# Optimization experiments

Hardware: AMD Instinct MI355X
Metric: run time of the kernel (lower is better)

The kernel has to match this reference:

```python
import jax, jax.numpy as jnp
import numpy as np

B, I, H, T = 64, 128, 256, 1024


def setup_inputs() -> dict:
    key = jax.random.key(0)
    ks = jax.random.split(key, 18)
    stdv = 1.0 / np.sqrt(H)  # reset_parameters: uniform(-1/sqrt(hidden), 1/sqrt(hidden))
    u = lambda k, shape: jax.random.uniform(k, shape, jnp.float32, -stdv, stdv)
    return dict(
        X=jax.random.normal(ks[0], (B, I, T), jnp.float32),
        Mask=jax.random.randint(ks[1], (B, I, T), 0, 2).astype(jnp.float32),
        Delta=jax.random.uniform(ks[2], (B, I, T), jnp.float32),
        x_mean=jnp.float32(0.0),
        Wdgx=u(ks[3], (I, I)), bdgx=u(ks[4], (I,)),
        Wdgh=u(ks[5], (H, I)), bdgh=u(ks[6], (H,)),
        Wxz=u(ks[7], (H, I)), Whz=u(ks[8], (H, H)), Wmz=u(ks[9], (H, I)), bmz=u(ks[10], (H,)),
        Wxr=u(ks[11], (H, I)), Whr=u(ks[12], (H, H)), Wmr=u(ks[13], (H, I)),
        Wxh=u(ks[14], (H, I)), Whh=u(ks[15], (H, H)), Wmh=u(ks[16], (H, I)), bmh=u(ks[17], (H,)),
    )


def _grud(X, Mask, Delta, x_mean, Wdgx, bdgx, Wdgh, bdgh, Wxz, Whz, Wmz, bmz,
          Wxr, Whr, Wmr, Wxh, Whh, Wmh, bmh):
    # [B, I, T] -> time-major [T, B, I] for scan
    Xt = jnp.transpose(X, (2, 0, 1))
    Mt = jnp.transpose(Mask, (2, 0, 1))
    Dt = jnp.transpose(Delta, (2, 0, 1))

    def step(carry, xs):
        h, x_last = carry            # h: [B, H], x_last: [B, I]
        x, m, d = xs                 # each [B, I]
        gamma_x = jnp.exp(-jax.nn.relu(d @ Wdgx.T + bdgx))   # [B, I]
        gamma_h = jnp.exp(-jax.nn.relu(d @ Wdgh.T + bdgh))   # [B, H]
        x_last = jnp.where(m > 0, x, x_last)
        # faithful double imputation as in the torch source
        x1 = m * x + (1 - m) * (gamma_x * x + (1 - gamma_x) * x_mean)
        x2 = m * x1 + (1 - m) * (gamma_x * x_last + (1 - gamma_x) * x_mean)
        hd = gamma_h * h
        z = jax.nn.sigmoid(x2 @ Wxz.T + hd @ Whz.T + m @ Wmz.T + bmz)
        r = jax.nn.sigmoid(x2 @ Wxr.T + hd @ Whr.T + m @ Wmr.T)
        h_tilde = jnp.tanh(x2 @ Wxh.T + (r * hd) @ Whh.T + m @ Wmh.T + bmh)
        h_new = (1 - z) * hd + z * h_tilde
        return (h_new, x_last), h_new

    h0 = jnp.zeros((X.shape[0], Whz.shape[0]), X.dtype)      # Hidden_State buffer (zeros)
    xl0 = jnp.zeros((X.shape[0], X.shape[1]), X.dtype)       # X_last_obs buffer (zeros)
    _, hs = jax.lax.scan(step, (h0, xl0), (Xt, Mt, Dt))      # hs: [T, B, H]
    return jnp.transpose(hs, (1, 0, 2))                      # [B, T, H]


def reference(X, Mask, Delta, x_mean, Wdgx, bdgx, Wdgh, bdgh, Wxz, Whz, Wmz, bmz,
              Wxr, Whr, Wmr, Wxh, Whh, Wmh, bmh):
    return _grud(X, Mask, Delta, x_mean, Wdgx, bdgx, Wdgh, bdgh, Wxz, Whz, Wmz, bmz,
                 Wxr, Whr, Wmr, Wxh, Whh, Wmh, bmh)
```

## Files before the change

kernel.cpp:

```cpp
#include <hip/hip_runtime.h>
#include <cstdint>
#include <cstddef>

typedef _Float16 f16;
typedef _Float16 f16x8 __attribute__((ext_vector_type(8)));
typedef _Float16 f16x2 __attribute__((ext_vector_type(2)));
typedef float f32x4 __attribute__((ext_vector_type(4)));

#define B_ 64
#define I_ 128
#define H_ 256
#define T_ 1024
#define BT_ (B_*T_)

__device__ __forceinline__ uint32_t pack2_f16(float a, float b) {
  union { f16 h; uint16_t u; } ua, ub;
  ua.h = (f16)a; ub.h = (f16)b;
  return ((uint32_t)ub.u << 16) | (uint32_t)ua.u;
}

__device__ __forceinline__ float fdot2_u(uint32_t w, uint32_t x, float acc) {
  union { uint32_t u; f16x2 h; } uw, ux;
  uw.u = w; ux.u = x;
  return __builtin_amdgcn_fdot2(uw.h, ux.h, acc, false);
}

__device__ __forceinline__ float tanh_stable(float s) {
  float a = fabsf(s);
  float e = __expf(-2.f * a);
  float t = (1.f - e) * __fdividef(1.f, 1.f + e);
  return s < 0.f ? -t : t;
}

__device__ __forceinline__ float sigmoidf(float s) {
  return __fdividef(1.f, 1.f + __expf(-s));
}

__device__ __forceinline__ f16x8 load_frag(const f16* row, int k0, int g4) {
  union { uint32_t u[4]; f16x8 h; } r;
  const uint32_t* p0 = (const uint32_t*)(row + k0 + g4);
  const uint32_t* p1 = (const uint32_t*)(row + k0 + 16 + g4);
  r.u[0] = p0[0]; r.u[1] = p0[1];
  r.u[2] = p1[0]; r.u[3] = p1[1];
  return r.h;
}

__global__ void k_transpose_d(const float* __restrict__ D, f16* __restrict__ Dt) {
  __shared__ float tile[64][65];
  int t0 = blockIdx.x * 64, i0 = blockIdx.y * 64, b = blockIdx.z;
  int tx = threadIdx.x, ty = threadIdx.y;
  #pragma unroll
  for (int r = 0; r < 16; ++r) {
    int il = ty + r * 4;
    tile[il][tx] = D[((size_t)(b * I_ + i0 + il)) * T_ + t0 + tx];
  }
  __syncthreads();
  #pragma unroll
  for (int r = 0; r < 16; ++r) {
    int tl = ty + r * 4;
    Dt[((size_t)(b * T_ + t0 + tl)) * I_ + i0 + tx] = (f16)tile[tx][tl];
  }
}

__global__ void k_prep(const float* __restrict__ Wdgx, const float* __restrict__ bdgx,
                       const float* __restrict__ Wdgh, const float* __restrict__ bdgh,
                       const float* __restrict__ Wxz, const float* __restrict__ Whz,
                       const float* __restrict__ Wmz, const float* __restrict__ bmz,
                       const float* __restrict__ Wxr, const float* __restrict__ Whr,
                       const float* __restrict__ Wmr,
                       const float* __restrict__ Wxh, const float* __restrict__ Whh,
                       const float* __restrict__ Wmh, const float* __restrict__ bmh,
                       f16* __restrict__ Wg, float* __restrict__ bg,
                       f16* __restrict__ W3, float* __restrict__ b3,
                       uint32_t* __restrict__ blobR, uint32_t* __restrict__ blobZ,
                       uint32_t* __restrict__ blobH) {
  int tid = blockIdx.x * blockDim.x + threadIdx.x;
  int nth = gridDim.x * blockDim.x;
  for (int idx = tid; idx < 384 * 128; idx += nth) {
    int j = idx >> 7, k = idx & 127;
    float v = (j < 128) ? Wdgx[j * 128 + k] : Wdgh[(j - 128) * 128 + k];
    Wg[idx] = (f16)v;
  }
  for (int j = tid; j < 384; j += nth) bg[j] = (j < 128) ? bdgx[j] : bdgh[j - 128];
  for (int idx = tid; idx < 768 * 256; idx += nth) {
    int j = idx >> 8, c = idx & 255;
    const float* Wx = (j < 256) ? Wxz : ((j < 512) ? Wxr : Wxh);
    const float* Wm = (j < 256) ? Wmz : ((j < 512) ? Wmr : Wmh);
    int jj = j & 255;
    float v = (c < 128) ? Wx[jj * 128 + c] : Wm[jj * 128 + (c - 128)];
    W3[idx] = (f16)v;
  }
  for (int j = tid; j < 768; j += nth)
    b3[j] = (j < 256) ? bmz[j] : ((j < 512) ? 0.0f : bmh[j - 512]);
  for (int idx = tid; idx < 64 * 512; idx += nth) {
    int c = idx >> 9, th = idx & 511;
    int rr = c >> 5, cc = c & 31;
    int ks = th >> 7, rg = th & 127;
    int row = rg * 2 + rr;
    int k = ks * 64 + cc * 2;
    blobR[idx] = pack2_f16(Whr[row * 256 + k], Whr[row * 256 + k + 1]);
    blobZ[idx] = pack2_f16(Whz[row * 256 + k], Whz[row * 256 + k + 1]);
    blobH[idx] = pack2_f16(Whh[row * 256 + k], Whh[row * 256 + k + 1]);
  }
}

__global__ __launch_bounds__(256) void k_gemm1(const f16* __restrict__ A,
                                               const f16* __restrict__ W,
                                               const float* __restrict__ bias,
                                               float* __restrict__ Gx,
                                               f16* __restrict__ Gh) {
  __shared__ __align__(16) f16 As[64][136];
  __shared__ __align__(16) f16 Ws[128][136];
  int m0 = blockIdx.x * 64, n0 = blockIdx.y * 128;
  int tid = threadIdx.x;
  {
    int r = tid >> 2, sgm = tid & 3;
    const uint4* src = (const uint4*)(A + (size_t)(m0 + r) * 128 + sgm * 32);
    uint4* dst = (uint4*)(&As[r][sgm * 32]);
    #pragma unroll
    for (int q = 0; q < 4; ++q) dst[q] = src[q];
  }
  {
    int r = tid >> 1, hf = tid & 1;
    const uint4* src = (const uint4*)(W + (size_t)(n0 + r) * 128 + hf * 64);
    uint4* dst = (uint4*)(&Ws[r][hf * 64]);
    #pragma unroll
    for (int q = 0; q < 8; ++q) dst[q] = src[q];
  }
  __syncthreads();
  int w = tid >> 6, l = tid & 63;
  int lr = l & 15, g4 = (l >> 4) * 4;
  f32x4 acc[8] = {};
  #pragma unroll
  for (int kk = 0; kk < 4; ++kk) {
    int k0 = kk * 32;
    f16x8 a = load_frag(&As[w * 16 + lr][0], k0, g4);
    #pragma unroll
    for (int nt = 0; nt < 8; ++nt) {
      f16x8 bf = load_frag(&Ws[nt * 16 + lr][0], k0, g4);
      acc[nt] = __builtin_amdgcn_mfma_f32_16x16x32_f16(a, bf, acc[nt], 0, 0, 0);
    }
  }
  int row4 = (l >> 4) * 4;
  #pragma unroll
  for (int nt = 0; nt < 8; ++nt) {
    int n = n0 + nt * 16 + lr;
    float bv = bias[n];
    #pragma unroll
    for (int reg = 0; reg < 4; ++reg) {
      int m = m0 + w * 16 + row4 + reg;
      float s = acc[nt][reg] + bv;
      float g = __expf(-fmaxf(s, 0.0f));
      if (n < 128) Gx[(size_t)m * 128 + n] = g;
      else         Gh[(size_t)m * 256 + (n - 128)] = (f16)g;
    }
  }
}

__global__ __launch_bounds__(256) void k_gemm3(const f16* __restrict__ A,
                                               const f16* __restrict__ W,
                                               const float* __restrict__ bias,
                                               f16* __restrict__ P) {
  __shared__ __align__(16) f16 As[64][136];
  __shared__ __align__(16) f16 Ws[128][136];
  int m0 = blockIdx.x * 64, n0 = blockIdx.y * 128;
  int tid = threadIdx.x;
  int w = tid >> 6, l = tid & 63, lr = l & 15, g4 = (l >> 4) * 4;
  f32x4 acc[8] = {};
  for (int kh = 0; kh < 2; ++kh) {
    {
      int r = tid >> 2, sgm = tid & 3;
      const uint4* src = (const uint4*)(A + (size_t)(m0 + r) * 256 + kh * 128 + sgm * 32);
      uint4* dst = (uint4*)(&As[r][sgm * 32]);
      #pragma unroll
      for (int q = 0; q < 4; ++q) dst[q] = src[q];
    }
    {
      int r = tid >> 1, hf = tid & 1;
      const uint4* src = (const uint4*)(W + (size_t)(n0 + r) * 256 + kh * 128 + hf * 64);
      uint4* dst = (uint4*)(&Ws[r][hf * 64]);
      #pragma unroll
      for (int q = 0; q < 8; ++q) dst[q] = src[q];
    }
    __syncthreads();
    #pragma unroll
    for (int kk = 0; kk < 4; ++kk) {
      int k0 = kk * 32;
      f16x8 a = load_frag(&As[w * 16 + lr][0], k0, g4);
      #pragma unroll
      for (int nt = 0; nt < 8; ++nt) {
        f16x8 bf = load_frag(&Ws[nt * 16 + lr][0], k0, g4);
        acc[nt] = __builtin_amdgcn_mfma_f32_16x16x32_f16(a, bf, acc[nt], 0, 0, 0);
      }
    }
    __syncthreads();
  }
  int row4 = (l >> 4) * 4;
  #pragma unroll
  for (int nt = 0; nt < 8; ++nt) {
    int n = n0 + nt * 16 + lr;
    float bv = bias[n];
    #pragma unroll
    for (int reg = 0; reg < 4; ++reg) {
      int m = m0 + w * 16 + row4 + reg;
      P[(size_t)m * 768 + n] = (f16)(acc[nt][reg] + bv);
    }
  }
}

__global__ void k_seg(const float* __restrict__ X, const float* __restrict__ M,
                      float* __restrict__ segX, float* __restrict__ segF) {
  int b = blockIdx.x, s = blockIdx.y, i = threadIdx.x;
  const float* xr = X + ((size_t)(b * I_ + i)) * T_ + s * 128;
  const float* mr = M + ((size_t)(b * I_ + i)) * T_ + s * 128;
  float last = 0.f, seen = 0.f;
  for (int t = 0; t < 128; ++t) {
    float m = mr[t];
    float x = xr[t];
    if (m > 0.f) { last = x; seen = 1.f; }
  }
  segX[((size_t)(b * I_ + i)) * 8 + s] = last;
  segF[((size_t)(b * I_ + i)) * 8 + s] = seen;
}

__global__ void k_x2(const float* __restrict__ X, const float* __restrict__ M,
                     const float* __restrict__ Gx, const float* __restrict__ xmean_p,
                     const float* __restrict__ segX, const float* __restrict__ segF,
                     f16* __restrict__ AC) {
  int b = blockIdx.x, s = blockIdx.y, i = threadIdx.x;
  float xm = xmean_p[0];
  float xl = 0.f;
  const float* sF = segF + ((size_t)(b * I_ + i)) * 8;
  const float* sX = segX + ((size_t)(b * I_ + i)) * 8;
  for (int p = 0; p < s; ++p) { if (sF[p] > 0.f) xl = sX[p]; }
  const float* xr = X + ((size_t)(b * I_ + i)) * T_;
  const float* mr = M + ((size_t)(b * I_ + i)) * T_;
  for (int tl = 0; tl < 128; ++tl) {
    int t = s * 128 + tl;
    float x = xr[t], m = mr[t];
    float gx = Gx[((size_t)(b * T_ + t)) * I_ + i];
    if (m > 0.f) xl = x;
    float x1 = m * x + (1.f - m) * (gx * x + (1.f - gx) * xm);
    float x2 = m * x1 + (1.f - m) * (gx * xl + (1.f - gx) * xm);
    size_t o = ((size_t)(b * T_ + t)) * 256;
    AC[o + i] = (f16)x2;
    AC[o + 128 + i] = (f16)m;
  }
}

__global__ __launch_bounds__(512, 2) void k_recur(
    const f16* __restrict__ Gh, const f16* __restrict__ P,
    const uint32_t* __restrict__ blobR, const uint32_t* __restrict__ blobZ,
    const uint32_t* __restrict__ blobH, float* __restrict__ out) {
  __shared__ __align__(16) f16 hdh[256];
  __shared__ __align__(16) f16 rhdh[256];
  __shared__ __align__(16) float partR[4][256];
  __shared__ __align__(16) float partZ[4][256];
  __shared__ __align__(16) float partH[4][256];
  int tid = threadIdx.x;
  int b = blockIdx.x;
  int ks = tid >> 7, rg = tid & 127;
  bool lo = tid < 256;

  uint32_t wR[64], wZ[64], wH[64];
  #pragma unroll
  for (int c = 0; c < 64; ++c) wR[c] = blobR[c * 512 + tid];
  #pragma unroll
  for (int c = 0; c < 64; ++c) wZ[c] = blobZ[c * 512 + tid];
  #pragma unroll
  for (int c = 0; c < 64; ++c) wH[c] = blobH[c * 512 + tid];

  const f16* gbase = Gh + (size_t)b * T_ * 256;
  const f16* pbase = P + (size_t)b * T_ * 768;
  const f16* ghp = gbase + 2 * 256 + tid;
  const f16* pzp = pbase + 768 + tid;
  const f16* php = pbase + 768 + 512 + tid;
  float* outp = out + (size_t)b * T_ * 256 + tid;

  float h = 0.f, hd = 0.f;
  float pzr_c = (float)pzp[-768];
  float ph_c  = lo ? (float)php[-768] : 0.f;
  float gh_u  = lo ? (float)gbase[256 + tid] : 0.f;
  if (lo) hdh[tid] = (f16)0.f;
  __syncthreads();

  for (int it = 0; it < T_; ++it) {
    float pzr_n = 0.f, ph_n = 0.f, gh_n = 0.f;
    if (it + 1 < T_) {
      pzr_n = (float)pzp[0];
      if (lo) ph_n = (float)php[0];
    }
    if (lo && it + 2 < T_) gh_n = (float)ghp[0];
    pzp += 768; php += 768; ghp += 256;

    const uint32_t* hdu = (const uint32_t*)hdh;
    {
      float a0 = 0.f, a1 = 0.f;
      #pragma unroll
      for (int cc = 0; cc < 32; ++cc) {
        uint32_t hv = hdu[ks * 32 + cc];
        a0 = fdot2_u(wR[cc], hv, a0);
        a1 = fdot2_u(wR[32 + cc], hv, a1);
      }
      partR[ks][rg * 2 + 0] = a0;
      partR[ks][rg * 2 + 1] = a1;
    }
    __syncthreads();
    if (!lo) {
      int tr = tid - 256;
      float s = pzr_c + partR[0][tr] + partR[1][tr] + partR[2][tr] + partR[3][tr];
      float r = sigmoidf(s);
      rhdh[tr] = (f16)(r * (float)hdh[tr]);
    }
    __syncthreads();
    {
      const uint32_t* rhu = (const uint32_t*)rhdh;
      float z0 = 0.f, z1 = 0.f, t0 = 0.f, t1 = 0.f;
      #pragma unroll
      for (int cc = 0; cc < 32; ++cc) {
        uint32_t hv = hdu[ks * 32 + cc];
        uint32_t rv = rhu[ks * 32 + cc];
        z0 = fdot2_u(wZ[cc], hv, z0);
        z1 = fdot2_u(wZ[32 + cc], hv, z1);
        t0 = fdot2_u(wH[cc], rv, t0);
        t1 = fdot2_u(wH[32 + cc], rv, t1);
      }
      partZ[ks][rg * 2 + 0] = z0;
      partZ[ks][rg * 2 + 1] = z1;
      partH[ks][rg * 2 + 0] = t0;
      partH[ks][rg * 2 + 1] = t1;
    }
    __syncthreads();
    if (lo) {
      float sz = pzr_c + partZ[0][tid] + partZ[1][tid] + partZ[2][tid] + partZ[3][tid];
      float z = sigmoidf(sz);
      float s2 = ph_c + partH[0][tid] + partH[1][tid] + partH[2][tid] + partH[3][tid];
      float ht = tanh_stable(s2);
      float hnew = (1.f - z) * hd + z * ht;
      outp[0] = hnew;
      hd = gh_u * hnew;
      hdh[tid] = (f16)hd;
      outp += 256;
    }
    pzr_c = pzr_n; ph_c = ph_n; gh_u = gh_n;
    __syncthreads();
  }
}

static constexpr size_t OFF_P  = 0;
static constexpr size_t OFF_DT = 0;
static constexpr size_t OFF_GX = 100663296;
static constexpr size_t OFF_GH = OFF_GX + 33554432;
static constexpr size_t OFF_AC = OFF_GH + 33554432;
static constexpr size_t OFF_WG = OFF_AC + 33554432;
static constexpr size_t OFF_BG = OFF_WG + 98304;
static constexpr size_t OFF_W3 = OFF_BG + 1536;
static constexpr size_t OFF_B3 = OFF_W3 + 393216;
static constexpr size_t OFF_BR = OFF_B3 + 3072;
static constexpr size_t OFF_BZ = OFF_BR + 131072;
static constexpr size_t OFF_BH = OFF_BZ + 131072;
static constexpr size_t OFF_SX = OFF_BH + 131072;
static constexpr size_t OFF_SF = OFF_SX + 262144;
static constexpr size_t WS_TOTAL = OFF_SF + 262144;

extern "C" void kernel_launch(void* const* d_in, const int* in_sizes, int n_in,
                              void* d_out, int out_size, void* d_ws, size_t ws_size,
                              hipStream_t stream) {
  const float* X    = (const float*)d_in[0];
  const float* Mask = (const float*)d_in[1];
  const float* Delta= (const float*)d_in[2];
  const float* xm   = (const float*)d_in[3];
  const float* Wdgx = (const float*)d_in[4];
  const float* bdgx = (const float*)d_in[5];
  const float* Wdgh = (const float*)d_in[6];
  const float* bdgh = (const float*)d_in[7];
  const float* Wxz  = (const float*)d_in[8];
  const float* Whz  = (const float*)d_in[9];
  const float* Wmz  = (const float*)d_in[10];
  const float* bmz  = (const float*)d_in[11];
  const float* Wxr  = (const float*)d_in[12];
  const float* Whr  = (const float*)d_in[13];
  const float* Wmr  = (const float*)d_in[14];
  const float* Wxh  = (const float*)d_in[15];
  const float* Whh  = (const float*)d_in[16];
  const float* Wmh  = (const float*)d_in[17];
  const float* bmh  = (const float*)d_in[18];
  float* out = (float*)d_out;
  char* ws = (char*)d_ws;
  if (ws_size < WS_TOTAL) return;

  f16*      Dt   = (f16*)(ws + OFF_DT);
  f16*      P    = (f16*)(ws + OFF_P);
  float*    Gx   = (float*)(ws + OFF_GX);
  f16*      Gh   = (f16*)(ws + OFF_GH);
  f16*      AC   = (f16*)(ws + OFF_AC);
  f16*      Wg   = (f16*)(ws + OFF_WG);
  float*    bg   = (float*)(ws + OFF_BG);
  f16*      W3   = (f16*)(ws + OFF_W3);
  float*    b3   = (float*)(ws + OFF_B3);
  uint32_t* blR  = (uint32_t*)(ws + OFF_BR);
  uint32_t* blZ  = (uint32_t*)(ws + OFF_BZ);
  uint32_t* blH  = (uint32_t*)(ws + OFF_BH);
  float*    segX = (float*)(ws + OFF_SX);
  float*    segF = (float*)(ws + OFF_SF);

  k_prep<<<dim3(64), dim3(256), 0, stream>>>(Wdgx, bdgx, Wdgh, bdgh, Wxz, Whz, Wmz, bmz,
                                             Wxr, Whr, Wmr, Wxh, Whh, Wmh, bmh,
                                             Wg, bg, W3, b3, blR, blZ, blH);
  k_transpose_d<<<dim3(16, 2, 64), dim3(64, 4), 0, stream>>>(Delta, Dt);
  k_gemm1<<<dim3(1024, 3), dim3(256), 0, stream>>>(Dt, Wg, bg, Gx, Gh);
  k_seg<<<dim3(64, 8), dim3(128), 0, stream>>>(X, Mask, segX, segF);
  k_x2<<<dim3(64, 8), dim3(128), 0, stream>>>(X, Mask, Gx, xm, segX, segF, AC);
  k_gemm3<<<dim3(1024, 6), dim3(256), 0, stream>>>(AC, W3, b3, P);
  k_recur<<<dim3(64), dim3(512), 0, stream>>>(Gh, P, blR, blZ, blH, out);
}
```

Before: 2.271 ms.

## Force one block per CU and vectorize LDS hidden-state reads in recurrence

The recurrent kernel now uses launch bounds of one block per CU and a large dummy LDS allocation, so each of the 64 batch blocks lands on its own CU and gets more registers. Hidden-state reads from LDS are widened to 128-bit loads, with sched_barrier hints to control instruction interleaving. The r-gate matvec is moved ahead of the global prefetch loads, and partial sums are stored as float2. The cost is wasted LDS and dependence on the scheduler hints behaving well.

```diff
diff --git a/kernel.cpp b/kernel.cpp
--- a/kernel.cpp
+++ b/kernel.cpp
@@ -248,7 +248,7 @@
   }
 }
 
-__global__ __launch_bounds__(512, 2) void k_recur(
+__global__ __launch_bounds__(512, 1) void k_recur8(
     const f16* __restrict__ Gh, const f16* __restrict__ P,
     const uint32_t* __restrict__ blobR, const uint32_t* __restrict__ blobZ,
     const uint32_t* __restrict__ blobH, float* __restrict__ out) {
@@ -257,10 +257,13 @@
   __shared__ __align__(16) float partR[4][256];
   __shared__ __align__(16) float partZ[4][256];
   __shared__ __align__(16) float partH[4][256];
+  __shared__ __align__(16) uint32_t lds_forcer[22528];
   int tid = threadIdx.x;
   int b = blockIdx.x;
   int ks = tid >> 7, rg = tid & 127;
   bool lo = tid < 256;
+
+  ((volatile uint32_t*)lds_forcer)[tid] = 0u;
 
   uint32_t wR[64], wZ[64], wH[64];
   #pragma unroll
@@ -277,14 +280,32 @@
   const f16* php = pbase + 768 + 512 + tid;
   float* outp = out + (size_t)b * T_ * 256 + tid;
 
-  float h = 0.f, hd = 0.f;
-  float pzr_c = (float)pzp[-768];
-  float ph_c  = lo ? (float)php[-768] : 0.f;
+  float hd = 0.f, z = 0.f;
+  float pzr_c = (float)pbase[tid];
+  float ph_c  = lo ? (float)pbase[512 + tid] : 0.f;
   float gh_u  = lo ? (float)gbase[256 + tid] : 0.f;
   if (lo) hdh[tid] = (f16)0.f;
   __syncthreads();
 
   for (int it = 0; it < T_; ++it) {
+    const uint4* hd4 = (const uint4*)hdh;
+    {
+      float a0 = 0.f, a1 = 0.f;
+      #pragma unroll
+      for (int c4 = 0; c4 < 8; ++c4) {
+        uint4 hv = hd4[ks * 8 + c4];
+        a0 = fdot2_u(wR[c4 * 4 + 0], hv.x, a0);
+        a0 = fdot2_u(wR[c4 * 4 + 1], hv.y, a0);
+        a0 = fdot2_u(wR[c4 * 4 + 2], hv.z, a0);
+        a0 = fdot2_u(wR[c4 * 4 + 3], hv.w, a0);
+        a1 = fdot2_u(wR[32 + c4 * 4 + 0], hv.x, a1);
+        a1 = fdot2_u(wR[32 + c4 * 4 + 1], hv.y, a1);
+        a1 = fdot2_u(wR[32 + c4 * 4 + 2], hv.z, a1);
+        a1 = fdot2_u(wR[32 + c4 * 4 + 3], hv.w, a1);
+        if (c4 & 1) __builtin_amdgcn_sched_barrier(0);
+      }
+      *(float2*)(&partR[ks][rg * 2]) = make_float2(a0, a1);
+    }
     float pzr_n = 0.f, ph_n = 0.f, gh_n = 0.f;
     if (it + 1 < T_) {
       pzr_n = (float)pzp[0];
@@ -292,55 +313,54 @@
     }
     if (lo && it + 2 < T_) gh_n = (float)ghp[0];
     pzp += 768; php += 768; ghp += 256;
-
-    const uint32_t* hdu = (const uint32_t*)hdh;
+    __syncthreads();
+    if (!lo) {
+      int row = tid - 256;
+      float s = pzr_c + partR[0][row] + partR[1][row] + partR[2][row] + partR[3][row];
+      float r = sigmoidf(s);
+      rhdh[row] = (f16)(r * (float)hdh[row]);
+    }
+    __syncthreads();
     {
-      float a0 = 0.f, a1 = 0.f;
-      #pragma unroll
-      for (int cc = 0; cc < 32; ++cc) {
-        uint32_t hv = hdu[ks * 32 + cc];
-        a0 = fdot2_u(wR[cc], hv, a0);
-        a1 = fdot2_u(wR[32 + cc], hv, a1);
-      }
-      partR[ks][rg * 2 + 0] = a0;
-      partR[ks][rg * 2 + 1] = a1;
-    }
-    __syncthreads();
-    if (!lo) {
-      int tr = tid - 256;
-      float s = pzr_c + partR[0][tr] + partR[1][tr] + partR[2][tr] + partR[3][tr];
-      float r = sigmoidf(s);
-      rhdh[tr] = (f16)(r * (float)hdh[tr]);
-    }
-    __syncthreads();
-    {
-      const uint32_t* rhu = (const uint32_t*)rhdh;
+      const uint4* rh4 = (const uint4*)rhdh;
       float z0 = 0.f, z1 = 0.f, t0 = 0.f, t1 = 0.f;
       #pragma unroll
-      for (int cc = 0; cc < 32; ++cc) {
-        uint32_t hv = hdu[ks * 32 + cc];
-        uint32_t rv = rhu[ks * 32 + cc];
-        z0 = fdot2_u(wZ[cc], hv, z0);
-        z1 = fdot2_u(wZ[32 + cc], hv, z1);
-        t0 = fdot2_u(wH[cc], rv, t0);
-        t1 = fdot2_u(wH[32 + cc], rv, t1);
+      for (int c4 = 0; c4 < 8; ++c4) {
+        uint4 hv = hd4[ks * 8 + c4];
+        uint4 rv = rh4[ks * 8 + c4];
+        z0 = fdot2_u(wZ[c4 * 4 + 0], hv.x, z0);
+        z0 = fdot2_u(wZ[c4 * 4 + 1], hv.y, z0);
+        z0 = fdot2_u(wZ[c4 * 4 + 2], hv.z, z0);
+        z0 = fdot2_u(wZ[c4 * 4 + 3], hv.w, z0);
+        z1 = fdot2_u(wZ[32 + c4 * 4 + 0], hv.x, z1);
+        z1 = fdot2_u(wZ[32 + c4 * 4 + 1], hv.y, z1);
+        z1 = fdot2_u(wZ[32 + c4 * 4 + 2], hv.z, z1);
+        z1 = fdot2_u(wZ[32 + c4 * 4 + 3], hv.w, z1);
+        t0 = fdot2_u(wH[c4 * 4 + 0], rv.x, t0);
+        t0 = fdot2_u(wH[c4 * 4 + 1], rv.y, t0);
+        t0 = fdot2_u(wH[c4 * 4 + 2], rv.z, t0);
+        t0 = fdot2_u(wH[c4 * 4 + 3], rv.w, t0);
+        t1 = fdot2_u(wH[32 + c4 * 4 + 0], rv.x, t1);
+        t1 = fdot2_u(wH[32 + c4 * 4 + 1], rv.y, t1);
+        t1 = fdot2_u(wH[32 + c4 * 4 + 2], rv.z, t1);
+        t1 = fdot2_u(wH[32 + c4 * 4 + 3], rv.w, t1);
+        if (c4 & 1) __builtin_amdgcn_sched_barrier(0);
       }
-      partZ[ks][rg * 2 + 0] = z0;
-      partZ[ks][rg * 2 + 1] = z1;
-      partH[ks][rg * 2 + 0] = t0;
-      partH[ks][rg * 2 + 1] = t1;
+      *(float2*)(&partZ[ks][rg * 2]) = make_float2(z0, z1);
+      *(float2*)(&partH[ks][rg * 2]) = make_float2(t0, t1);
     }
     __syncthreads();
     if (lo) {
       float sz = pzr_c + partZ[0][tid] + partZ[1][tid] + partZ[2][tid] + partZ[3][tid];
-      float z = sigmoidf(sz);
+      float zc = sigmoidf(sz);
       float s2 = ph_c + partH[0][tid] + partH[1][tid] + partH[2][tid] + partH[3][tid];
       float ht = tanh_stable(s2);
-      float hnew = (1.f - z) * hd + z * ht;
+      float hnew = (1.f - zc) * hd + zc * ht;
       outp[0] = hnew;
+      outp += 256;
       hd = gh_u * hnew;
       hdh[tid] = (f16)hd;
-      outp += 256;
+      z = zc;
     }
     pzr_c = pzr_n; ph_c = ph_n; gh_u = gh_n;
     __syncthreads();
@@ -412,5 +432,5 @@
   k_seg<<<dim3(64, 8), dim3(128), 0, stream>>>(X, Mask, segX, segF);
   k_x2<<<dim3(64, 8), dim3(128), 0, stream>>>(X, Mask, Gx, xm, segX, segF, AC);
   k_gemm3<<<dim3(1024, 6), dim3(256), 0, stream>>>(AC, W3, b3, P);
-  k_recur<<<dim3(64), dim3(512), 0, stream>>>(Gh, P, blR, blZ, blH, out);
-}
+  k_recur8<<<dim3(64), dim3(512), 0, stream>>>(Gh, P, blR, blZ, blH, out);
+}
```

Result: slower. 2.317 ms (+2.0%).

## Move Whz to LDS, compute z with r, shrink per-step critical path

Applied to the files above, without the earlier changes.

The recurrent kernel now computes the z-gate dot products in the same phase as the r-gate, since both depend only on hd. This shortens the serial chain after r is known to just the candidate-state matvec. To fit registers, Whz weights move into LDS as packed uint4 blobs, and the last 8 columns of Whh go to LDS as well. hd and rhd are read as 128-bit vectors with sched_barriers to control instruction interleaving. The trade is extra LDS bandwidth per step and about 144KB of LDS use, which may limit residency, in exchange for fewer dependent phases and lower register pressure.

```diff
diff --git a/kernel.cpp b/kernel.cpp
--- a/kernel.cpp
+++ b/kernel.cpp
@@ -72,8 +72,8 @@
                        const float* __restrict__ Wmh, const float* __restrict__ bmh,
                        f16* __restrict__ Wg, float* __restrict__ bg,
                        f16* __restrict__ W3, float* __restrict__ b3,
-                       uint32_t* __restrict__ blobR, uint32_t* __restrict__ blobZ,
-                       uint32_t* __restrict__ blobH) {
+                       uint32_t* __restrict__ blobR, uint32_t* __restrict__ blobHrg,
+                       uint32_t* __restrict__ blobZ4, uint32_t* __restrict__ blobHl4) {
   int tid = blockIdx.x * blockDim.x + threadIdx.x;
   int nth = gridDim.x * blockDim.x;
   for (int idx = tid; idx < 384 * 128; idx += nth) {
@@ -93,14 +93,37 @@
   for (int j = tid; j < 768; j += nth)
     b3[j] = (j < 256) ? bmz[j] : ((j < 512) ? 0.0f : bmh[j - 512]);
   for (int idx = tid; idx < 64 * 512; idx += nth) {
-    int c = idx >> 9, th = idx & 511;
+    int c = idx >> 9, t = idx & 511;
     int rr = c >> 5, cc = c & 31;
-    int ks = th >> 7, rg = th & 127;
+    int ks = t >> 7, rg = t & 127;
     int row = rg * 2 + rr;
     int k = ks * 64 + cc * 2;
     blobR[idx] = pack2_f16(Whr[row * 256 + k], Whr[row * 256 + k + 1]);
-    blobZ[idx] = pack2_f16(Whz[row * 256 + k], Whz[row * 256 + k + 1]);
-    blobH[idx] = pack2_f16(Whh[row * 256 + k], Whh[row * 256 + k + 1]);
+  }
+  for (int idx = tid; idx < 56 * 512; idx += nth) {
+    int c = idx >> 9, t = idx & 511;
+    int rr = (c >= 28) ? 1 : 0, cc = c - rr * 28;
+    int ks = t >> 7, rg = t & 127;
+    int row = rg * 2 + rr;
+    int k = ks * 64 + cc * 2;
+    blobHrg[idx] = pack2_f16(Whh[row * 256 + k], Whh[row * 256 + k + 1]);
+  }
+  for (int idx = tid; idx < 16 * 512 * 4; idx += nth) {
+    int q = idx & 3, r = idx >> 2;
+    int t = r & 511, c4 = r >> 9;
+    int rr = c4 >> 3, qq = c4 & 7;
+    int ks = t >> 7, rg = t & 127;
+    int row = rg * 2 + rr;
+    int k = ks * 64 + qq * 8 + q * 2;
+    blobZ4[idx] = pack2_f16(Whz[row * 256 + k], Whz[row * 256 + k + 1]);
+  }
+  for (int idx = tid; idx < 2 * 512 * 4; idx += nth) {
+    int q = idx & 3, r = idx >> 2;
+    int t = r & 511, rr = r >> 9;
+    int ks = t >> 7, rg = t & 127;
+    int row = rg * 2 + rr;
+    int k = ks * 64 + 56 + q * 2;
+    blobHl4[idx] = pack2_f16(Whh[row * 256 + k], Whh[row * 256 + k + 1]);
   }
 }
 
@@ -248,27 +271,32 @@
   }
 }
 
-__global__ __launch_bounds__(512, 2) void k_recur(
+__global__ __launch_bounds__(512, 2) void k_recur10(
     const f16* __restrict__ Gh, const f16* __restrict__ P,
-    const uint32_t* __restrict__ blobR, const uint32_t* __restrict__ blobZ,
-    const uint32_t* __restrict__ blobH, float* __restrict__ out) {
+    const uint32_t* __restrict__ blobR, const uint32_t* __restrict__ blobHrg,
+    const uint32_t* __restrict__ blobZ4, const uint32_t* __restrict__ blobHl4,
+    float* __restrict__ out) {
+  __shared__ __align__(16) uint4 whzl[16 * 512];
+  __shared__ __align__(16) uint4 whhl[2 * 512];
+  __shared__ __align__(16) float partR[4][256];
+  __shared__ __align__(16) float partZ[4][256];
   __shared__ __align__(16) f16 hdh[256];
   __shared__ __align__(16) f16 rhdh[256];
-  __shared__ __align__(16) float partR[4][256];
-  __shared__ __align__(16) float partZ[4][256];
-  __shared__ __align__(16) float partH[4][256];
   int tid = threadIdx.x;
   int b = blockIdx.x;
   int ks = tid >> 7, rg = tid & 127;
   bool lo = tid < 256;
 
-  uint32_t wR[64], wZ[64], wH[64];
+  #pragma unroll
+  for (int i = 0; i < 16; ++i) whzl[i * 512 + tid] = ((const uint4*)blobZ4)[i * 512 + tid];
+  #pragma unroll
+  for (int i = 0; i < 2; ++i)  whhl[i * 512 + tid] = ((const uint4*)blobHl4)[i * 512 + tid];
+
+  uint32_t wR[64], wH[56];
   #pragma unroll
   for (int c = 0; c < 64; ++c) wR[c] = blobR[c * 512 + tid];
   #pragma unroll
-  for (int c = 0; c < 64; ++c) wZ[c] = blobZ[c * 512 + tid];
-  #pragma unroll
-  for (int c = 0; c < 64; ++c) wH[c] = blobH[c * 512 + tid];
+  for (int c = 0; c < 56; ++c) wH[c] = blobHrg[c * 512 + tid];
 
   const f16* gbase = Gh + (size_t)b * T_ * 256;
   const f16* pbase = P + (size_t)b * T_ * 768;
@@ -277,14 +305,45 @@
   const f16* php = pbase + 768 + 512 + tid;
   float* outp = out + (size_t)b * T_ * 256 + tid;
 
-  float h = 0.f, hd = 0.f;
-  float pzr_c = (float)pzp[-768];
-  float ph_c  = lo ? (float)php[-768] : 0.f;
+  float hd_own = 0.f, z_reg = 0.f;
+  float pzr_c = (float)pbase[tid];
+  float ph_c  = lo ? (float)pbase[512 + tid] : 0.f;
   float gh_u  = lo ? (float)gbase[256 + tid] : 0.f;
   if (lo) hdh[tid] = (f16)0.f;
   __syncthreads();
 
   for (int it = 0; it < T_; ++it) {
+    {
+      const uint4* hd4 = (const uint4*)hdh;
+      float r0 = 0.f, r1 = 0.f, z0 = 0.f, z1 = 0.f;
+      #pragma unroll
+      for (int c4 = 0; c4 < 8; ++c4) {
+        uint4 hv = hd4[ks * 8 + c4];
+        r0 = fdot2_u(wR[c4 * 4 + 0], hv.x, r0);
+        r0 = fdot2_u(wR[c4 * 4 + 1], hv.y, r0);
+        r0 = fdot2_u(wR[c4 * 4 + 2], hv.z, r0);
+        r0 = fdot2_u(wR[c4 * 4 + 3], hv.w, r0);
+        r1 = fdot2_u(wR[32 + c4 * 4 + 0], hv.x, r1);
+        r1 = fdot2_u(wR[32 + c4 * 4 + 1], hv.y, r1);
+        r1 = fdot2_u(wR[32 + c4 * 4 + 2], hv.z, r1);
+        r1 = fdot2_u(wR[32 + c4 * 4 + 3], hv.w, r1);
+        uint4 wz0 = whzl[c4 * 512 + tid];
+        z0 = fdot2_u(wz0.x, hv.x, z0);
+        z0 = fdot2_u(wz0.y, hv.y, z0);
+        z0 = fdot2_u(wz0.z, hv.z, z0);
+        z0 = fdot2_u(wz0.w, hv.w, z0);
+        uint4 wz1 = whzl[(8 + c4) * 512 + tid];
+        z1 = fdot2_u(wz1.x, hv.x, z1);
+        z1 = fdot2_u(wz1.y, hv.y, z1);
+        z1 = fdot2_u(wz1.z, hv.z, z1);
+        z1 = fdot2_u(wz1.w, hv.w, z1);
+        if (c4 & 1) __builtin_amdgcn_sched_barrier(0);
+      }
+      partR[ks][rg * 2 + 0] = r0;
+      partR[ks][rg * 2 + 1] = r1;
+      partZ[ks][rg * 2 + 0] = z0;
+      partZ[ks][rg * 2 + 1] = z1;
+    }
     float pzr_n = 0.f, ph_n = 0.f, gh_n = 0.f;
     if (it + 1 < T_) {
       pzr_n = (float)pzp[0];
@@ -292,55 +351,56 @@
     }
     if (lo && it + 2 < T_) gh_n = (float)ghp[0];
     pzp += 768; php += 768; ghp += 256;
-
-    const uint32_t* hdu = (const uint32_t*)hdh;
+    __syncthreads();
+    if (lo) {
+      z_reg = sigmoidf(pzr_c + partZ[0][tid] + partZ[1][tid] + partZ[2][tid] + partZ[3][tid]);
+    } else {
+      int row = tid - 256;
+      float s = pzr_c + partR[0][row] + partR[1][row] + partR[2][row] + partR[3][row];
+      rhdh[row] = (f16)(sigmoidf(s) * (float)hdh[row]);
+    }
+    __syncthreads();
     {
-      float a0 = 0.f, a1 = 0.f;
+      const uint4* rh4 = (const uint4*)rhdh;
+      float h0 = 0.f, h1 = 0.f;
       #pragma unroll
-      for (int cc = 0; cc < 32; ++cc) {
-        uint32_t hv = hdu[ks * 32 + cc];
-        a0 = fdot2_u(wR[cc], hv, a0);
-        a1 = fdot2_u(wR[32 + cc], hv, a1);
+      for (int c4 = 0; c4 < 7; ++c4) {
+        uint4 rv = rh4[ks * 8 + c4];
+        h0 = fdot2_u(wH[c4 * 4 + 0], rv.x, h0);
+        h0 = fdot2_u(wH[c4 * 4 + 1], rv.y, h0);
+        h0 = fdot2_u(wH[c4 * 4 + 2], rv.z, h0);
+        h0 = fdot2_u(wH[c4 * 4 + 3], rv.w, h0);
+        h1 = fdot2_u(wH[28 + c4 * 4 + 0], rv.x, h1);
+        h1 = fdot2_u(wH[28 + c4 * 4 + 1], rv.y, h1);
+        h1 = fdot2_u(wH[28 + c4 * 4 + 2], rv.z, h1);
+        h1 = fdot2_u(wH[28 + c4 * 4 + 3], rv.w, h1);
+        if (c4 & 1) __builtin_amdgcn_sched_barrier(0);
       }
-      partR[ks][rg * 2 + 0] = a0;
-      partR[ks][rg * 2 + 1] = a1;
-    }
-    __syncthreads();
-    if (!lo) {
-      int tr = tid - 256;
-      float s = pzr_c + partR[0][tr] + partR[1][tr] + partR[2][tr] + partR[3][tr];
-      float r = sigmoidf(s);
-      rhdh[tr] = (f16)(r * (float)hdh[tr]);
-    }
-    __syncthreads();
-    {
-      const uint32_t* rhu = (const uint32_t*)rhdh;
-      float z0 = 0.f, z1 = 0.f, t0 = 0.f, t1 = 0.f;
-      #pragma unroll
-      for (int cc = 0; cc < 32; ++cc) {
-        uint32_t hv = hdu[ks * 32 + cc];
-        uint32_t rv = rhu[ks * 32 + cc];
-        z0 = fdot2_u(wZ[cc], hv, z0);
-        z1 = fdot2_u(wZ[32 + cc], hv, z1);
-        t0 = fdot2_u(wH[cc], rv, t0);
-        t1 = fdot2_u(wH[32 + cc], rv, t1);
+      {
+        uint4 rv = rh4[ks * 8 + 7];
+        uint4 wh0 = whhl[0 * 512 + tid];
+        h0 = fdot2_u(wh0.x, rv.x, h0);
+        h0 = fdot2_u(wh0.y, rv.y, h0);
+        h0 = fdot2_u(wh0.z, rv.z, h0);
+        h0 = fdot2_u(wh0.w, rv.w, h0);
+        uint4 wh1 = whhl[1 * 512 + tid];
+        h1 = fdot2_u(wh1.x, rv.x, h1);
+        h1 = fdot2_u(wh1.y, rv.y, h1);
+        h1 = fdot2_u(wh1.z, rv.z, h1);
+        h1 = fdot2_u(wh1.w, rv.w, h1);
       }
-      partZ[ks][rg * 2 + 0] = z0;
-      partZ[ks][rg * 2 + 1] = z1;
-      partH[ks][rg * 2 + 0] = t0;
-      partH[ks][rg * 2 + 1] = t1;
+      partR[ks][rg * 2 + 0] = h0;
+      partR[ks][rg * 2 + 1] = h1;
     }
     __syncthreads();
     if (lo) {
-      float sz = pzr_c + partZ[0][tid] + partZ[1][tid] + partZ[2][tid] + partZ[3][tid];
-      float z = sigmoidf(sz);
-      float s2 = ph_c + partH[0][tid] + partH[1][tid] + partH[2][tid] + partH[3][tid];
+      float s2 = ph_c + partR[0][tid] + partR[1][tid] + partR[2][tid] + partR[3][tid];
       float ht = tanh_stable(s2);
-      float hnew = (1.f - z) * hd + z * ht;
+      float hnew = (1.f - z_reg) * hd_own + z_reg * ht;
       outp[0] = hnew;
-      hd = gh_u * hnew;
-      hdh[tid] = (f16)hd;
       outp += 256;
+      hd_own = gh_u * hnew;
+      hdh[tid] = (f16)hd_own;
     }
     pzr_c = pzr_n; ph_c = ph_n; gh_u = gh_n;
     __syncthreads();
@@ -357,9 +417,10 @@
 static constexpr size_t OFF_W3 = OFF_BG + 1536;
 static constexpr size_t OFF_B3 = OFF_W3 + 393216;
 static constexpr size_t OFF_BR = OFF_B3 + 3072;
-static constexpr size_t OFF_BZ = OFF_BR + 131072;
-static constexpr size_t OFF_BH = OFF_BZ + 131072;
-static constexpr size_t OFF_SX = OFF_BH + 131072;
+static constexpr size_t OFF_BH = OFF_BR + 131072;
+static constexpr size_t OFF_BZ = OFF_BH + 114688;
+static constexpr size_t OFF_BL = OFF_BZ + 131072;
+static constexpr size_t OFF_SX = OFF_BL + 16384;
 static constexpr size_t OFF_SF = OFF_SX + 262144;
 static constexpr size_t WS_TOTAL = OFF_SF + 262144;
 
@@ -399,18 +460,19 @@
   f16*      W3   = (f16*)(ws + OFF_W3);
   float*    b3   = (float*)(ws + OFF_B3);
   uint32_t* blR  = (uint32_t*)(ws + OFF_BR);
+  uint32_t* blH  = (uint32_t*)(ws + OFF_BH);
   uint32_t* blZ  = (uint32_t*)(ws + OFF_BZ);
-  uint32_t* blH  = (uint32_t*)(ws + OFF_BH);
+  uint32_t* blL  = (uint32_t*)(ws + OFF_BL);
   float*    segX = (float*)(ws + OFF_SX);
   float*    segF = (float*)(ws + OFF_SF);
 
   k_prep<<<dim3(64), dim3(256), 0, stream>>>(Wdgx, bdgx, Wdgh, bdgh, Wxz, Whz, Wmz, bmz,
                                              Wxr, Whr, Wmr, Wxh, Whh, Wmh, bmh,
-                                             Wg, bg, W3, b3, blR, blZ, blH);
+                                             Wg, bg, W3, b3, blR, blH, blZ, blL);
   k_transpose_d<<<dim3(16, 2, 64), dim3(64, 4), 0, stream>>>(Delta, Dt);
   k_gemm1<<<dim3(1024, 3), dim3(256), 0, stream>>>(Dt, Wg, bg, Gx, Gh);
   k_seg<<<dim3(64, 8), dim3(128), 0, stream>>>(X, Mask, segX, segF);
   k_x2<<<dim3(64, 8), dim3(128), 0, stream>>>(X, Mask, Gx, xm, segX, segF, AC);
   k_gemm3<<<dim3(1024, 6), dim3(256), 0, stream>>>(AC, W3, b3, P);
-  k_recur<<<dim3(64), dim3(512), 0, stream>>>(Gh, P, blR, blZ, blH, out);
-}
+  k_recur10<<<dim3(64), dim3(512), 0, stream>>>(Gh, P, blR, blH, blZ, blL, out);
+}
```

New measurement: 2.203 ms, median of 2. 1.03x faster.
